# Performance work log

Measured on AMD Instinct MI355X. Metric: run time of the kernel, lower is better.

## Reference

```python
import jax, jax.numpy as jnp
import numpy as np

NEG_SLOPE = 0.2  # PyG GATConv default negative_slope
NUM_GRAPHS = 64
N, E, F_IN = 50000, 800000, 128


def _gat(x, src, dst, W, a_s, a_d, b, concat):
    # PyG GATConv: h = x W (per head); e_ij = leaky_relu(a_s.h_j + a_d.h_i);
    # softmax over incoming edges of each dst node; out_i = sum_j alpha_ij h_j
    n = x.shape[0]
    H, C = a_s.shape
    h = (x @ W).reshape(n, H, C)                     # [N,H,C]
    es = jnp.einsum('nhc,hc->nh', h, a_s)            # [N,H]
    ed = jnp.einsum('nhc,hc->nh', h, a_d)
    e = jax.nn.leaky_relu(es[src] + ed[dst], NEG_SLOPE)   # [E,H]
    m = jax.ops.segment_max(e, dst, num_segments=n)       # per-dst max (stable softmax)
    ex = jnp.exp(e - m[dst])
    den = jax.ops.segment_sum(ex, dst, num_segments=n)
    alpha = ex / den[dst]                                 # [E,H]
    out = jax.ops.segment_sum(h[src] * alpha[:, :, None], dst, num_segments=n)  # [N,H,C]
    if concat:
        return out.reshape(n, H * C) + b
    return out.mean(axis=1) + b


def setup_inputs() -> dict:
    key = jax.random.key(0)
    ks = jax.random.split(key, 10)
    x = jax.random.normal(ks[0], (N, F_IN), jnp.float32)
    edge_index = jax.random.randint(ks[1], (2, E), 0, N, dtype=jnp.int64)
    batch = jnp.sort(jax.random.randint(ks[2], (N,), 0, NUM_GRAPHS, dtype=jnp.int64))
    s1 = 1.0 / np.sqrt(F_IN)
    s2 = 1.0 / np.sqrt(256)
    return {
        'x': x,
        'edge_index': edge_index,
        'batch': batch,
        'W1': jax.random.normal(ks[3], (F_IN, 256), jnp.float32) * s1,
        'a_src1': jax.random.normal(ks[4], (4, 64), jnp.float32) * s2,
        'a_dst1': jax.random.normal(ks[5], (4, 64), jnp.float32) * s2,
        'b1': jnp.zeros((256,), jnp.float32),
        'W2': jax.random.normal(ks[6], (256, 128), jnp.float32) * s2,
        'a_src2': jax.random.normal(ks[7], (1, 128), jnp.float32) * (1.0 / np.sqrt(128)),
        'a_dst2': jax.random.normal(ks[8], (1, 128), jnp.float32) * (1.0 / np.sqrt(128)),
        'b2': jnp.zeros((128,), jnp.float32),
        'fc_w': jax.random.normal(ks[9], (128, 10), jnp.float32) * (1.0 / np.sqrt(128)),
        'fc_b': jnp.zeros((10,), jnp.float32),
    }


def reference(x, edge_index, batch, W1, a_src1, a_dst1, b1, W2, a_src2, a_dst2, b2, fc_w, fc_b):
    n = x.shape[0]
    loop = jnp.arange(n, dtype=edge_index.dtype)  # PyG add_self_loops=True
    src = jnp.concatenate([edge_index[0], loop])
    dst = jnp.concatenate([edge_index[1], loop])
    h = jax.nn.elu(_gat(x, src, dst, W1, a_src1, a_dst1, b1, True))   # dropout: eval mode -> identity
    h = jax.nn.elu(_gat(h, src, dst, W2, a_src2, a_dst2, b2, False))
    pooled = jax.ops.segment_sum(h, batch, num_segments=NUM_GRAPHS)
    cnt = jax.ops.segment_sum(jnp.ones((n,), h.dtype), batch, num_segments=NUM_GRAPHS)
    pooled = pooled / jnp.maximum(cnt, 1.0)[:, None]
    logits = pooled @ fc_w + fc_b
    return jax.nn.log_softmax(logits, axis=1)
```

## Files before the change

kernel.cpp:

```cpp
#include <hip/hip_runtime.h>
#include <math.h>

#define N_NODES 50000
#define N_PAD   50048
#define N_EDGES 800000
#define E_TOT   (N_EDGES + N_NODES)
#define NG 64
#define POOL_CHUNK 64
#define CAP 48
#define NBKT 512
#define BNODES 98
#define RCAP 24
#define FILL_CHUNK 2048
#define GEMM1_BLOCKS 3128
#define FILL_BLOCKS  391
#define PH1_DIAG (FILL_BLOCKS * 8)
#define PH1_TOTAL (GEMM1_BLOCKS + FILL_BLOCKS)

typedef short short8 __attribute__((ext_vector_type(8)));
typedef float floatx4 __attribute__((ext_vector_type(4)));
typedef float floatx2 __attribute__((ext_vector_type(2)));

__device__ inline short f2bf(float f) {
    union { float f; unsigned u; } v; v.f = f;
    unsigned r = v.u + 0x7fff + ((v.u >> 16) & 1);
    return (short)(r >> 16);
}
__device__ inline float bf2f(short s) {
    union { float f; unsigned u; } v;
    v.u = ((unsigned)(unsigned short)s) << 16;
    return v.f;
}

__device__ inline unsigned f2fp8(float f) {
    union { float f; unsigned u; } v; v.f = f;
    unsigned s = v.u & 0x80000000u;
    unsigned au = v.u & 0x7fffffffu;
    if (au > 0x43E00000u) au = 0x43E00000u;
    unsigned r = au + 0x7ffffu + ((au >> 20) & 1);
    int e8 = (int)(r >> 23) - 120;
    unsigned m3 = (r >> 20) & 7;
    unsigned code;
    if (e8 <= 0) code = 0;
    else if (e8 > 15) code = 0x7e;
    else code = ((unsigned)e8 << 3) | m3;
    return (s >> 24) | code;
}

__device__ inline float leaky_exp(float t) {
    t = t > 0.f ? t : 0.2f * t;
    return __expf(t);
}


__global__ __launch_bounds__(256) void phase1_kernel(const float* __restrict__ x,
                                                     const float* __restrict__ W1,
                                                     const float* __restrict__ a_s,
                                                     const float* __restrict__ a_d,
                                                     const int* __restrict__ ei,
                                                     unsigned short* __restrict__ gcnt,
                                                     unsigned* __restrict__ gb2,
                                                     unsigned char* __restrict__ C8,
                                                     float* __restrict__ es,
                                                     float* __restrict__ ed,
                                                     const float* __restrict__ W2,
                                                     const float* __restrict__ as2,
                                                     const float* __restrict__ ad2,
                                                     float* __restrict__ ws2,
                                                     float* __restrict__ wd2) {
    __shared__ short bs[64][136];
    __shared__ int hist[NBKT];
    int bid = blockIdx.x;
    int tid = threadIdx.x;

    if (bid == PH1_TOTAL) {
        int k = tid;
        float s = 0.f, d = 0.f;
        for (int c = 0; c < 128; c++) {
            float w = W2[k * 128 + c];
            s += w * as2[c];
            d += w * ad2[c];
        }
        ws2[k] = s;
        wd2[k] = d;
        return;
    }

    int gb = -1, fb = -1;
    if (bid < PH1_DIAG) {
        int g = bid >> 3, r = bid & 7;
        if (r == (g & 7)) fb = g;
        else gb = g * 7 + (r > (g & 7) ? r - 1 : r);
    } else {
        gb = (PH1_DIAG - FILL_BLOCKS) + (bid - PH1_DIAG);
    }

    if (fb >= 0) {
        hist[tid] = 0; hist[tid + 256] = 0;
        __syncthreads();
        unsigned meta[8], pay[8];
        int e0 = fb * FILL_CHUNK;
#pragma unroll
        for (int j = 0; j < 8; j++) {
            int t = e0 + j * 256 + tid;
            if (t < N_EDGES) {
                int s = ei[t];
                int d = ei[N_EDGES + t];
                unsigned bkt = (unsigned)d / 98u;
                int dlow = d - (int)bkt * 98;
                int pos = atomicAdd(&hist[bkt], 1);
                meta[j] = (bkt << 16) | (unsigned)pos;
                pay[j] = ((unsigned)s << 9) | (unsigned)dlow;
            } else {
                meta[j] = 0xffffffffu;
            }
        }
        __syncthreads();
        {
            int c0h = hist[tid];        if (c0h > RCAP) c0h = RCAP;
            int c1h = hist[tid + 256];  if (c1h > RCAP) c1h = RCAP;
            gcnt[fb * NBKT + tid] = (unsigned short)c0h;
            gcnt[fb * NBKT + tid + 256] = (unsigned short)c1h;
        }
#pragma unroll
        for (int j = 0; j < 8; j++) {
            if (meta[j] != 0xffffffffu) {
                unsigned bkt = meta[j] >> 16;
                unsigned pos = meta[j] & 0xffffu;
                if (pos < RCAP)
                    gb2[((size_t)bkt * FILL_BLOCKS + fb) * RCAP + pos] = pay[j];
            }
        }
        return;
    }

    const int K = 128, N = 256;
    int head = gb & 3;
    int bx = gb >> 2;
    int c0 = head * 64;

    int tc = tid & 63;
    int tk0 = (tid >> 6) * 32;
    for (int k = tk0; k < tk0 + 32; k++)
        bs[tc][k] = f2bf(W1[k * 256 + c0 + tc]);
    __syncthreads();

    int wid = tid >> 6;
    int lane = tid & 63;
    int m0 = bx * 64 + wid * 16;
    int mr = lane & 15;
    int quad = lane >> 4;
    int kq = quad << 3;
    int arow = m0 + mr; if (arow > N_NODES - 1) arow = N_NODES - 1;
    const float* aptr = x + (size_t)arow * K + kq;
    floatx4 acc[4] = {{0.f,0.f,0.f,0.f},{0.f,0.f,0.f,0.f},{0.f,0.f,0.f,0.f},{0.f,0.f,0.f,0.f}};
    for (int k0 = 0; k0 < K; k0 += 32) {
        float4 f0 = *(const float4*)(aptr + k0);
        float4 f1 = *(const float4*)(aptr + k0 + 4);
        short8 a;
        a[0] = f2bf(f0.x); a[1] = f2bf(f0.y); a[2] = f2bf(f0.z); a[3] = f2bf(f0.w);
        a[4] = f2bf(f1.x); a[5] = f2bf(f1.y); a[6] = f2bf(f1.z); a[7] = f2bf(f1.w);
#pragma unroll
        for (int t = 0; t < 4; t++) {
            short8 b = *(const short8*)&bs[t * 16 + mr][kq + k0];
            acc[t] = __builtin_amdgcn_mfma_f32_16x16x32_bf16(a, b, acc[t], 0, 0, 0);
        }
    }
    float asv[4], adv[4];
#pragma unroll
    for (int t = 0; t < 4; t++) {
        asv[t] = a_s[c0 + t * 16 + mr];
        adv[t] = a_d[c0 + t * 16 + mr];
    }
    int orow = m0 + (quad << 2);
#pragma unroll
    for (int r = 0; r < 4; r++) {
        float ps = acc[0][r] * asv[0] + acc[1][r] * asv[1] + acc[2][r] * asv[2] + acc[3][r] * asv[3];
        float pd = acc[0][r] * adv[0] + acc[1][r] * adv[1] + acc[2][r] * adv[2] + acc[3][r] * adv[3];
#pragma unroll
        for (int off = 8; off >= 1; off >>= 1) {
            ps += __shfl_xor(ps, off);
            pd += __shfl_xor(pd, off);
        }
        if (mr == 0) {
            es[(orow + r) * 4 + head] = ps;
            ed[(orow + r) * 4 + head] = pd;
        }
    }
#pragma unroll
    for (int t = 0; t < 4; t++) {
        int ocol = c0 + t * 16 + mr;
#pragma unroll
        for (int r = 0; r < 4; r++) {
            C8[(size_t)(orow + r) * N + ocol] = (unsigned char)f2fp8(acc[t][r]);
        }
    }
}


__global__ __launch_bounds__(512) void binfill_kernel(const unsigned* __restrict__ gb2,
                                                      const unsigned short* __restrict__ gcnt,
                                                      unsigned short* __restrict__ col,
                                                      int* __restrict__ degT) {
    __shared__ unsigned colL[BNODES * CAP / 2];
    __shared__ int cnt[BNODES];
    __shared__ unsigned short cl[FILL_BLOCKS + 1];
    int b = blockIdx.x, tid = threadIdx.x;
    int nbase = b * BNODES;

    for (int i = tid; i < BNODES * CAP / 8; i += 512) ((uint4*)colL)[i] = make_uint4(0, 0, 0, 0);
    if (tid < FILL_BLOCKS) cl[tid] = gcnt[tid * NBKT + b];
    if (tid < BNODES) cnt[tid] = (nbase + tid < N_NODES) ? 1 : 0;
    __syncthreads();

    if (tid < BNODES) {
        int nn = nbase + tid;
        if (nn < N_NODES) ((unsigned short*)colL)[tid * CAP] = (unsigned short)nn;
    }
    const uint4* src4 = (const uint4*)(gb2 + (size_t)b * FILL_BLOCKS * RCAP);
    for (int r = tid; r < FILL_BLOCKS * RCAP / 4; r += 512) {
        int blk = r / 6;
        int q = r - blk * 6;
        int c = cl[blk];
        if (q * 4 < c) {
            uint4 v = src4[r];
            unsigned vv[4] = {v.x, v.y, v.z, v.w};
#pragma unroll
            for (int j = 0; j < 4; j++) {
                if (q * 4 + j < c) {
                    unsigned p = vv[j];
                    int dlow = (int)(p & 511u);
                    int s = (int)(p >> 9);
                    int sp = atomicAdd(&cnt[dlow], 1);
                    if (sp < CAP) ((unsigned short*)colL)[dlow * CAP + sp] = (unsigned short)s;
                }
            }
        }
    }
    __syncthreads();

    uint4* cb = (uint4*)(col + (size_t)b * BNODES * CAP);
    for (int i = tid; i < BNODES * CAP / 8; i += 512) cb[i] = ((uint4*)colL)[i];
    if (tid < BNODES) {
        int nn = nbase + tid;
        if (nn < N_NODES) degT[nn] = cnt[tid];
    }
}


__global__ __launch_bounds__(256) void gather1_kernel(const unsigned char* __restrict__ h8,
                                                      const int* __restrict__ degT,
                                                      const unsigned short* __restrict__ col,
                                                      const float* __restrict__ es,
                                                      const float* __restrict__ ed,
                                                      const float* __restrict__ bias,
                                                      const float* __restrict__ ws2,
                                                      const float* __restrict__ wd2,
                                                      short* __restrict__ out,
                                                      float* __restrict__ es2,
                                                      float* __restrict__ ed2) {
    __shared__ float wlds[4][CAP * 4];
    __shared__ unsigned short ilds[4][CAP];
    int tid = threadIdx.x;
    int wid = tid >> 6;
    int n = __builtin_amdgcn_readfirstlane(blockIdx.x * 4 + wid);
    int l = tid & 63;
    int hh = l >> 4;
    int cnt = degT[n]; cnt = cnt < CAP ? cnt : CAP;
    int cnt8 = (cnt + 7) & ~7;

    if (l < cnt8) ilds[wid][l] = col[n * CAP + l];

    {
        int eA = l >> 2;
        int hA = l & 3;
        float edvA = ed[n * 4 + hA];
#pragma unroll
        for (int p = 0; p < 3; p++) {
            int e = p * 16 + eA;
            if (e < cnt8) {
                int s = ilds[wid][e];
                float w = (e < cnt) ? leaky_exp(es[s * 4 + hA] + edvA) : 0.f;
                wlds[wid][e * 4 + hA] = w;
            }
        }
    }

    float ax = 0.f, ay = 0.f, az = 0.f, aw = 0.f, den = 0.f;
    for (int eb = 0; eb < cnt8; eb += 8) {
        int idx[8];
#pragma unroll
        for (int j = 0; j < 8; j++) idx[j] = ilds[wid][eb + j];
        float wv[8];
#pragma unroll
        for (int j = 0; j < 8; j++) wv[j] = wlds[wid][(eb + j) * 4 + hh];
        unsigned hv[8];
#pragma unroll
        for (int j = 0; j < 8; j++)
            hv[j] = *(const unsigned*)&h8[(size_t)idx[j] * 256 + l * 4];
#pragma unroll
        for (int j = 0; j < 8; j++) {
            floatx2 lo = __builtin_amdgcn_cvt_pk_f32_fp8(hv[j], false);
            floatx2 hi = __builtin_amdgcn_cvt_pk_f32_fp8(hv[j], true);
            den += wv[j];
            ax += wv[j] * lo[0];
            ay += wv[j] * lo[1];
            az += wv[j] * hi[0];
            aw += wv[j] * hi[1];
        }
    }
    float inv = 1.0f / den;
    float4 bb = *(const float4*)&bias[l * 4];
    float o0 = ax * inv + bb.x;
    float o1 = ay * inv + bb.y;
    float o2 = az * inv + bb.z;
    float o3 = aw * inv + bb.w;
    o0 = o0 > 0.f ? o0 : __expf(o0) - 1.f;
    o1 = o1 > 0.f ? o1 : __expf(o1) - 1.f;
    o2 = o2 > 0.f ? o2 : __expf(o2) - 1.f;
    o3 = o3 > 0.f ? o3 : __expf(o3) - 1.f;
    short4 ob;
    ob.x = f2bf(o0); ob.y = f2bf(o1); ob.z = f2bf(o2); ob.w = f2bf(o3);
    *(short4*)&out[(size_t)n * 256 + l * 4] = ob;

    float4 s4 = *(const float4*)&ws2[l * 4];
    float4 d4 = *(const float4*)&wd2[l * 4];
    float ps = o0 * s4.x + o1 * s4.y + o2 * s4.z + o3 * s4.w;
    float pd = o0 * d4.x + o1 * d4.y + o2 * d4.z + o3 * d4.w;
#pragma unroll
    for (int off = 32; off >= 1; off >>= 1) {
        ps += __shfl_xor(ps, off);
        pd += __shfl_xor(pd, off);
    }
    if (l == 0) {
        es2[n] = ps;
        ed2[n] = pd;
    }
}


__global__ __launch_bounds__(256) void gemm2_kernel(const short* __restrict__ A,
                                                    const float* __restrict__ W2,
                                                    unsigned char* __restrict__ C8) {
    __shared__ short bs[64][264];
    const int K = 256, N = 128;
    int tid = threadIdx.x;
    int by = blockIdx.y;
    int c0 = by * 64;

    int tc = tid & 63;
    int tk0 = (tid >> 6) * 64;
    for (int k = tk0; k < tk0 + 64; k++)
        bs[tc][k] = f2bf(W2[k * 128 + c0 + tc]);
    __syncthreads();

    int wid = tid >> 6;
    int lane = tid & 63;
    int m0 = blockIdx.x * 64 + wid * 16;
    int mr = lane & 15;
    int quad = lane >> 4;
    int kq = quad << 3;
    const short* arow = A + (size_t)(m0 + mr) * K + kq;
    floatx4 acc[4] = {{0.f,0.f,0.f,0.f},{0.f,0.f,0.f,0.f},{0.f,0.f,0.f,0.f},{0.f,0.f,0.f,0.f}};
    for (int k0 = 0; k0 < K; k0 += 32) {
        short8 a = *(const short8*)(arow + k0);
#pragma unroll
        for (int t = 0; t < 4; t++) {
            short8 b = *(const short8*)&bs[t * 16 + mr][kq + k0];
            acc[t] = __builtin_amdgcn_mfma_f32_16x16x32_bf16(a, b, acc[t], 0, 0, 0);
        }
    }
    int orow = m0 + (quad << 2);
#pragma unroll
    for (int t = 0; t < 4; t++) {
        int ocol = c0 + t * 16 + mr;
#pragma unroll
        for (int r = 0; r < 4; r++) {
            C8[(size_t)(orow + r) * N + ocol] = (unsigned char)f2fp8(acc[t][r]);
        }
    }
}


__global__ __launch_bounds__(256) void gather2_kernel(const unsigned char* __restrict__ h8,
                                                      const int* __restrict__ deg,
                                                      const unsigned short* __restrict__ col,
                                                      const float* __restrict__ es2,
                                                      const float* __restrict__ ed2,
                                                      const float* __restrict__ bias,
                                                      short* __restrict__ out) {
    __shared__ float wlds[4][CAP];
    int tid = threadIdx.x;
    int wid = tid >> 6;
    int n = __builtin_amdgcn_readfirstlane(blockIdx.x * 4 + wid);
    int l = tid & 63;
    int cnt = deg[n]; cnt = cnt < CAP ? cnt : CAP;
    int cnt8 = (cnt + 7) & ~7;

    {
        float edv = ed2[n];
        if (l < cnt8) {
            int s = col[n * CAP + l];
            float w = (l < cnt) ? leaky_exp(es2[s] + edv) : 0.f;
            wlds[wid][l] = w;
        }
    }

    const unsigned int* cp = (const unsigned int*)(col + n * CAP);
    float ax = 0.f, ay = 0.f, den = 0.f;
    for (int eb = 0; eb < cnt8; eb += 8) {
        unsigned int cw0 = cp[(eb >> 1) + 0];
        unsigned int cw1 = cp[(eb >> 1) + 1];
        unsigned int cw2 = cp[(eb >> 1) + 2];
        unsigned int cw3 = cp[(eb >> 1) + 3];
        int idx[8];
        idx[0] = cw0 & 0xffff; idx[1] = cw0 >> 16;
        idx[2] = cw1 & 0xffff; idx[3] = cw1 >> 16;
        idx[4] = cw2 & 0xffff; idx[5] = cw2 >> 16;
        idx[6] = cw3 & 0xffff; idx[7] = cw3 >> 16;
        float wv[8];
#pragma unroll
        for (int j = 0; j < 8; j++) wv[j] = wlds[wid][eb + j];
        unsigned hv[8];
#pragma unroll
        for (int j = 0; j < 8; j++)
            hv[j] = *(const unsigned short*)&h8[(size_t)idx[j] * 128 + l * 2];
#pragma unroll
        for (int j = 0; j < 8; j++) {
            floatx2 lo = __builtin_amdgcn_cvt_pk_f32_fp8(hv[j], false);
            den += wv[j];
            ax += wv[j] * lo[0];
            ay += wv[j] * lo[1];
        }
    }
    float inv = 1.0f / den;
    float2 bb = *(const float2*)&bias[l * 2];
    float o0 = ax * inv + bb.x;
    float o1 = ay * inv + bb.y;
    o0 = o0 > 0.f ? o0 : __expf(o0) - 1.f;
    o1 = o1 > 0.f ? o1 : __expf(o1) - 1.f;
    short2 ob;
    ob.x = f2bf(o0); ob.y = f2bf(o1);
    *(short2*)&out[(size_t)n * 128 + l * 2] = ob;
}


__global__ __launch_bounds__(128) void pool1_kernel(const short* __restrict__ h,
                                                    const int* __restrict__ batch,
                                                    float* __restrict__ pooled) {
    int c = threadIdx.x;
    int n0 = blockIdx.x * POOL_CHUNK;
    int n1 = n0 + POOL_CHUNK;
    if (n1 > N_NODES) n1 = N_NODES;
    if (n0 >= n1) return;
    float acc = 0.f;
    int g = batch[n0];
    for (int n = n0; n < n1; n++) {
        int bg = batch[n];
        if (bg != g) {
            atomicAdd(&pooled[g * 128 + c], acc);
            acc = 0.f;
            g = bg;
        }
        acc += bf2f(h[n * 128 + c]);
    }
    atomicAdd(&pooled[g * 128 + c], acc);
}


__global__ void fc_kernel(const float* __restrict__ pooled, const int* __restrict__ batch,
                          const float* __restrict__ fcw, const float* __restrict__ fcb,
                          float* __restrict__ out) {
    int g = threadIdx.x;
    if (g >= NG) return;
    int lo = 0, hi = N_NODES;
    while (lo < hi) {
        int mid = (lo + hi) >> 1;
        if (batch[mid] < g) lo = mid + 1; else hi = mid;
    }
    int start = lo;
    lo = start; hi = N_NODES;
    while (lo < hi) {
        int mid = (lo + hi) >> 1;
        if (batch[mid] <= g) lo = mid + 1; else hi = mid;
    }
    int cnt = lo - start;
    float inv = 1.0f / (float)(cnt > 0 ? cnt : 1);

    float lg[10];
#pragma unroll
    for (int j = 0; j < 10; j++) lg[j] = fcb[j];
    for (int k = 0; k < 128; k++) {
        float p = pooled[g * 128 + k] * inv;
#pragma unroll
        for (int j = 0; j < 10; j++) lg[j] += p * fcw[k * 10 + j];
    }
    float m = lg[0];
#pragma unroll
    for (int j = 1; j < 10; j++) m = fmaxf(m, lg[j]);
    float se = 0.f;
#pragma unroll
    for (int j = 0; j < 10; j++) se += __expf(lg[j] - m);
    float lse = m + __logf(se);
#pragma unroll
    for (int j = 0; j < 10; j++) out[g * 10 + j] = lg[j] - lse;
}


extern "C" void kernel_launch(void* const* d_in, const int* in_sizes, int n_in,
                              void* d_out, int out_size, void* d_ws, size_t ws_size,
                              hipStream_t stream) {
    const float* x     = (const float*)d_in[0];
    const int*   ei    = (const int*)d_in[1];
    const int*   batch = (const int*)d_in[2];
    const float* W1    = (const float*)d_in[3];
    const float* as1   = (const float*)d_in[4];
    const float* ad1   = (const float*)d_in[5];
    const float* b1    = (const float*)d_in[6];
    const float* W2    = (const float*)d_in[7];
    const float* as2   = (const float*)d_in[8];
    const float* ad2   = (const float*)d_in[9];
    const float* b2    = (const float*)d_in[10];
    const float* fcw   = (const float*)d_in[11];
    const float* fcb   = (const float*)d_in[12];
    float* out = (float*)d_out;

    char* ws = (char*)d_ws;
    size_t off = 0;
    auto alloc = [&](size_t bytes) -> void* {
        void* p = ws + off;
        off = (off + bytes + 255) & ~(size_t)255;
        return p;
    };
    float* pooled        = (float*)alloc(NG * 128 * 4);
    int* degT            = (int*)alloc((size_t)N_PAD * 4);
    unsigned short* col  = (unsigned short*)alloc((size_t)NBKT * BNODES * CAP * 2);
    unsigned* gb2        = (unsigned*)alloc((size_t)NBKT * FILL_BLOCKS * RCAP * 4);
    unsigned short* gcnt = (unsigned short*)alloc((size_t)FILL_BLOCKS * NBKT * 2);
    float* es1           = (float*)alloc((size_t)N_PAD * 4 * 4);
    float* ed1           = (float*)alloc((size_t)N_PAD * 4 * 4);
    float* es2           = (float*)alloc((size_t)N_PAD * 4);
    float* ed2           = (float*)alloc((size_t)N_PAD * 4);
    float* ws2           = (float*)alloc(256 * 4);
    float* wd2           = (float*)alloc(256 * 4);
    unsigned char* h1    = (unsigned char*)alloc((size_t)N_PAD * 256);
    short* h1p           = (short*)alloc((size_t)N_PAD * 256 * 2);
    unsigned char* h2    = (unsigned char*)alloc((size_t)N_PAD * 128);
    short* h2p           = (short*)alloc((size_t)N_PAD * 128 * 2);

    hipMemsetAsync(pooled, 0, (size_t)NG * 128 * 4, stream);

    int ngrid = N_NODES / 4;

    phase1_kernel<<<PH1_TOTAL + 1, 256, 0, stream>>>(x, W1, as1, ad1, ei, gcnt, gb2, h1, es1, ed1,
                                                     W2, as2, ad2, ws2, wd2);
    binfill_kernel<<<NBKT, 512, 0, stream>>>(gb2, gcnt, col, degT);
    gather1_kernel<<<ngrid, 256, 0, stream>>>(h1, degT, col, es1, ed1, b1, ws2, wd2,
                                              h1p, es2, ed2);
    gemm2_kernel<<<dim3(N_PAD / 64, 2), 256, 0, stream>>>(h1p, W2, h2);
    gather2_kernel<<<ngrid, 256, 0, stream>>>(h2, degT, col, es2, ed2, b2, h2p);

    pool1_kernel<<<(N_NODES + POOL_CHUNK - 1) / POOL_CHUNK, 128, 0, stream>>>(h2p, batch, pooled);
    fc_kernel<<<1, 64, 0, stream>>>(pooled, batch, fcw, fcb, out);
}
```

Measured before the change: 237.9 us.

## Fuse mean-pool into gather2 and loop heads inside GEMM blocks

Layer-2 aggregation now accumulates per-graph sums directly, with a small LDS reduction and atomics into the pooled buffer. This removes the bf16 h2p intermediate, the separate pool kernel and the memset, whose zeroing moves into phase1's spare block. GEMM1 and GEMM2 blocks now load their A tile once and loop over heads or column halves, so the activations are read once instead of four or two times. The cost is fewer GEMM blocks, repeated W staging with extra barriers, and a gather2 where each wave handles eight nodes in sequence.

```diff
diff --git a/kernel.cpp b/kernel.cpp
--- a/kernel.cpp
+++ b/kernel.cpp
@@ -6,16 +6,15 @@
 #define N_EDGES 800000
 #define E_TOT   (N_EDGES + N_NODES)
 #define NG 64
-#define POOL_CHUNK 64
 #define CAP 48
 #define NBKT 512
 #define BNODES 98
 #define RCAP 24
 #define FILL_CHUNK 2048
-#define GEMM1_BLOCKS 3128
+#define GEMM1_BLOCKS 782
 #define FILL_BLOCKS  391
-#define PH1_DIAG (FILL_BLOCKS * 8)
 #define PH1_TOTAL (GEMM1_BLOCKS + FILL_BLOCKS)
+#define G2_NB 32
 
 typedef short short8 __attribute__((ext_vector_type(8)));
 typedef float floatx4 __attribute__((ext_vector_type(4)));
@@ -25,11 +24,6 @@
     union { float f; unsigned u; } v; v.f = f;
     unsigned r = v.u + 0x7fff + ((v.u >> 16) & 1);
     return (short)(r >> 16);
-}
-__device__ inline float bf2f(short s) {
-    union { float f; unsigned u; } v;
-    v.u = ((unsigned)(unsigned short)s) << 16;
-    return v.f;
 }
 
 __device__ inline unsigned f2fp8(float f) {
@@ -67,7 +61,8 @@
                                                      const float* __restrict__ as2,
                                                      const float* __restrict__ ad2,
                                                      float* __restrict__ ws2,
-                                                     float* __restrict__ wd2) {
+                                                     float* __restrict__ wd2,
+                                                     float* __restrict__ pooled) {
     __shared__ short bs[64][136];
     __shared__ int hist[NBKT];
     int bid = blockIdx.x;
@@ -83,16 +78,15 @@
         }
         ws2[k] = s;
         wd2[k] = d;
+        for (int i = tid; i < NG * 128; i += 256) pooled[i] = 0.f;
         return;
     }
 
     int gb = -1, fb = -1;
-    if (bid < PH1_DIAG) {
-        int g = bid >> 3, r = bid & 7;
-        if (r == (g & 7)) fb = g;
-        else gb = g * 7 + (r > (g & 7) ? r - 1 : r);
-    } else {
-        gb = (PH1_DIAG - FILL_BLOCKS) + (bid - PH1_DIAG);
+    {
+        int g3 = bid / 3, r3 = bid - g3 * 3;
+        if (r3 == 2) fb = g3;
+        else         gb = g3 * 2 + r3;
     }
 
     if (fb >= 0) {
@@ -135,64 +129,67 @@
     }
 
     const int K = 128, N = 256;
-    int head = gb & 3;
-    int bx = gb >> 2;
-    int c0 = head * 64;
-
     int tc = tid & 63;
-    int tk0 = (tid >> 6) * 32;
-    for (int k = tk0; k < tk0 + 32; k++)
-        bs[tc][k] = f2bf(W1[k * 256 + c0 + tc]);
-    __syncthreads();
-
+    int tk0s = (tid >> 6) * 32;
     int wid = tid >> 6;
     int lane = tid & 63;
-    int m0 = bx * 64 + wid * 16;
+    int m0 = gb * 64 + wid * 16;
     int mr = lane & 15;
     int quad = lane >> 4;
     int kq = quad << 3;
     int arow = m0 + mr; if (arow > N_NODES - 1) arow = N_NODES - 1;
     const float* aptr = x + (size_t)arow * K + kq;
-    floatx4 acc[4] = {{0.f,0.f,0.f,0.f},{0.f,0.f,0.f,0.f},{0.f,0.f,0.f,0.f},{0.f,0.f,0.f,0.f}};
-    for (int k0 = 0; k0 < K; k0 += 32) {
-        float4 f0 = *(const float4*)(aptr + k0);
-        float4 f1 = *(const float4*)(aptr + k0 + 4);
-        short8 a;
-        a[0] = f2bf(f0.x); a[1] = f2bf(f0.y); a[2] = f2bf(f0.z); a[3] = f2bf(f0.w);
-        a[4] = f2bf(f1.x); a[5] = f2bf(f1.y); a[6] = f2bf(f1.z); a[7] = f2bf(f1.w);
+    short8 a[4];
+#pragma unroll
+    for (int kk = 0; kk < 4; kk++) {
+        float4 f0 = *(const float4*)(aptr + kk * 32);
+        float4 f1 = *(const float4*)(aptr + kk * 32 + 4);
+        a[kk][0] = f2bf(f0.x); a[kk][1] = f2bf(f0.y); a[kk][2] = f2bf(f0.z); a[kk][3] = f2bf(f0.w);
+        a[kk][4] = f2bf(f1.x); a[kk][5] = f2bf(f1.y); a[kk][6] = f2bf(f1.z); a[kk][7] = f2bf(f1.w);
+    }
+    int orow = m0 + (quad << 2);
+    for (int head = 0; head < 4; head++) {
+        int c0 = head * 64;
+        if (head) __syncthreads();
+        for (int k = tk0s; k < tk0s + 32; k++)
+            bs[tc][k] = f2bf(W1[k * 256 + c0 + tc]);
+        __syncthreads();
+        floatx4 acc[4] = {{0.f,0.f,0.f,0.f},{0.f,0.f,0.f,0.f},{0.f,0.f,0.f,0.f},{0.f,0.f,0.f,0.f}};
+#pragma unroll
+        for (int kk = 0; kk < 4; kk++) {
+#pragma unroll
+            for (int t = 0; t < 4; t++) {
+                short8 b = *(const short8*)&bs[t * 16 + mr][kq + kk * 32];
+                acc[t] = __builtin_amdgcn_mfma_f32_16x16x32_bf16(a[kk], b, acc[t], 0, 0, 0);
+            }
+        }
+        float asv[4], adv[4];
 #pragma unroll
         for (int t = 0; t < 4; t++) {
-            short8 b = *(const short8*)&bs[t * 16 + mr][kq + k0];
-            acc[t] = __builtin_amdgcn_mfma_f32_16x16x32_bf16(a, b, acc[t], 0, 0, 0);
-        }
-    }
-    float asv[4], adv[4];
-#pragma unroll
-    for (int t = 0; t < 4; t++) {
-        asv[t] = a_s[c0 + t * 16 + mr];
-        adv[t] = a_d[c0 + t * 16 + mr];
-    }
-    int orow = m0 + (quad << 2);
-#pragma unroll
-    for (int r = 0; r < 4; r++) {
-        float ps = acc[0][r] * asv[0] + acc[1][r] * asv[1] + acc[2][r] * asv[2] + acc[3][r] * asv[3];
-        float pd = acc[0][r] * adv[0] + acc[1][r] * adv[1] + acc[2][r] * adv[2] + acc[3][r] * adv[3];
-#pragma unroll
-        for (int off = 8; off >= 1; off >>= 1) {
-            ps += __shfl_xor(ps, off);
-            pd += __shfl_xor(pd, off);
-        }
-        if (mr == 0) {
-            es[(orow + r) * 4 + head] = ps;
-            ed[(orow + r) * 4 + head] = pd;
-        }
-    }
-#pragma unroll
-    for (int t = 0; t < 4; t++) {
-        int ocol = c0 + t * 16 + mr;
+            asv[t] = a_s[c0 + t * 16 + mr];
+            adv[t] = a_d[c0 + t * 16 + mr];
+        }
 #pragma unroll
         for (int r = 0; r < 4; r++) {
-            C8[(size_t)(orow + r) * N + ocol] = (unsigned char)f2fp8(acc[t][r]);
+            float ps = acc[0][r] * asv[0] + acc[1][r] * asv[1] + acc[2][r] * asv[2] + acc[3][r] * asv[3];
+            float pd = acc[0][r] * adv[0] + acc[1][r] * adv[1] + acc[2][r] * adv[2] + acc[3][r] * adv[3];
+#pragma unroll
+            for (int off = 8; off >= 1; off >>= 1) {
+                ps += __shfl_xor(ps, off);
+                pd += __shfl_xor(pd, off);
+            }
+            if (mr == 0) {
+                es[(orow + r) * 4 + head] = ps;
+                ed[(orow + r) * 4 + head] = pd;
+            }
+        }
+#pragma unroll
+        for (int t = 0; t < 4; t++) {
+            int ocol = c0 + t * 16 + mr;
+#pragma unroll
+            for (int r = 0; r < 4; r++) {
+                C8[(size_t)(orow + r) * N + ocol] = (unsigned char)f2fp8(acc[t][r]);
+            }
         }
     }
 }
@@ -345,15 +342,8 @@
     __shared__ short bs[64][264];
     const int K = 256, N = 128;
     int tid = threadIdx.x;
-    int by = blockIdx.y;
-    int c0 = by * 64;
-
     int tc = tid & 63;
-    int tk0 = (tid >> 6) * 64;
-    for (int k = tk0; k < tk0 + 64; k++)
-        bs[tc][k] = f2bf(W2[k * 128 + c0 + tc]);
-    __syncthreads();
-
+    int tk0s = (tid >> 6) * 64;
     int wid = tid >> 6;
     int lane = tid & 63;
     int m0 = blockIdx.x * 64 + wid * 16;
@@ -361,22 +351,32 @@
     int quad = lane >> 4;
     int kq = quad << 3;
     const short* arow = A + (size_t)(m0 + mr) * K + kq;
-    floatx4 acc[4] = {{0.f,0.f,0.f,0.f},{0.f,0.f,0.f,0.f},{0.f,0.f,0.f,0.f},{0.f,0.f,0.f,0.f}};
-    for (int k0 = 0; k0 < K; k0 += 32) {
-        short8 a = *(const short8*)(arow + k0);
+    short8 a[8];
+#pragma unroll
+    for (int kk = 0; kk < 8; kk++) a[kk] = *(const short8*)(arow + kk * 32);
+    int orow = m0 + (quad << 2);
+    for (int by = 0; by < 2; by++) {
+        int c0 = by * 64;
+        if (by) __syncthreads();
+        for (int k = tk0s; k < tk0s + 64; k++)
+            bs[tc][k] = f2bf(W2[k * 128 + c0 + tc]);
+        __syncthreads();
+        floatx4 acc[4] = {{0.f,0.f,0.f,0.f},{0.f,0.f,0.f,0.f},{0.f,0.f,0.f,0.f},{0.f,0.f,0.f,0.f}};
+#pragma unroll
+        for (int kk = 0; kk < 8; kk++) {
+#pragma unroll
+            for (int t = 0; t < 4; t++) {
+                short8 b = *(const short8*)&bs[t * 16 + mr][kq + kk * 32];
+                acc[t] = __builtin_amdgcn_mfma_f32_16x16x32_bf16(a[kk], b, acc[t], 0, 0, 0);
+            }
+        }
 #pragma unroll
         for (int t = 0; t < 4; t++) {
-            short8 b = *(const short8*)&bs[t * 16 + mr][kq + k0];
-            acc[t] = __builtin_amdgcn_mfma_f32_16x16x32_bf16(a, b, acc[t], 0, 0, 0);
-        }
-    }
-    int orow = m0 + (quad << 2);
-#pragma unroll
-    for (int t = 0; t < 4; t++) {
-        int ocol = c0 + t * 16 + mr;
-#pragma unroll
-        for (int r = 0; r < 4; r++) {
-            C8[(size_t)(orow + r) * N + ocol] = (unsigned char)f2fp8(acc[t][r]);
+            int ocol = c0 + t * 16 + mr;
+#pragma unroll
+            for (int r = 0; r < 4; r++) {
+                C8[(size_t)(orow + r) * N + ocol] = (unsigned char)f2fp8(acc[t][r]);
+            }
         }
     }
 }
@@ -388,83 +388,107 @@
                                                       const float* __restrict__ es2,
                                                       const float* __restrict__ ed2,
                                                       const float* __restrict__ bias,
-                                                      short* __restrict__ out) {
+                                                      const int* __restrict__ batch,
+                                                      float* __restrict__ pooled) {
     __shared__ float wlds[4][CAP];
+    __shared__ float plds[8][128];
+    __shared__ int pg[8];
+    __shared__ int pcnt;
     int tid = threadIdx.x;
     int wid = tid >> 6;
-    int n = __builtin_amdgcn_readfirstlane(blockIdx.x * 4 + wid);
     int l = tid & 63;
-    int cnt = deg[n]; cnt = cnt < CAP ? cnt : CAP;
-    int cnt8 = (cnt + 7) & ~7;
-
-    {
-        float edv = ed2[n];
-        if (l < cnt8) {
-            int s = col[n * CAP + l];
-            float w = (l < cnt) ? leaky_exp(es2[s] + edv) : 0.f;
-            wlds[wid][l] = w;
-        }
-    }
-
-    const unsigned int* cp = (const unsigned int*)(col + n * CAP);
-    float ax = 0.f, ay = 0.f, den = 0.f;
-    for (int eb = 0; eb < cnt8; eb += 8) {
-        unsigned int cw0 = cp[(eb >> 1) + 0];
-        unsigned int cw1 = cp[(eb >> 1) + 1];
-        unsigned int cw2 = cp[(eb >> 1) + 2];
-        unsigned int cw3 = cp[(eb >> 1) + 3];
-        int idx[8];
-        idx[0] = cw0 & 0xffff; idx[1] = cw0 >> 16;
-        idx[2] = cw1 & 0xffff; idx[3] = cw1 >> 16;
-        idx[4] = cw2 & 0xffff; idx[5] = cw2 >> 16;
-        idx[6] = cw3 & 0xffff; idx[7] = cw3 >> 16;
-        float wv[8];
-#pragma unroll
-        for (int j = 0; j < 8; j++) wv[j] = wlds[wid][eb + j];
-        unsigned hv[8];
-#pragma unroll
-        for (int j = 0; j < 8; j++)
-            hv[j] = *(const unsigned short*)&h8[(size_t)idx[j] * 128 + l * 2];
-#pragma unroll
-        for (int j = 0; j < 8; j++) {
-            floatx2 lo = __builtin_amdgcn_cvt_pk_f32_fp8(hv[j], false);
-            den += wv[j];
-            ax += wv[j] * lo[0];
-            ay += wv[j] * lo[1];
-        }
-    }
-    float inv = 1.0f / den;
-    float2 bb = *(const float2*)&bias[l * 2];
-    float o0 = ax * inv + bb.x;
-    float o1 = ay * inv + bb.y;
-    o0 = o0 > 0.f ? o0 : __expf(o0) - 1.f;
-    o1 = o1 > 0.f ? o1 : __expf(o1) - 1.f;
-    short2 ob;
-    ob.x = f2bf(o0); ob.y = f2bf(o1);
-    *(short2*)&out[(size_t)n * 128 + l * 2] = ob;
-}
-
-
-__global__ __launch_bounds__(128) void pool1_kernel(const short* __restrict__ h,
-                                                    const int* __restrict__ batch,
-                                                    float* __restrict__ pooled) {
-    int c = threadIdx.x;
-    int n0 = blockIdx.x * POOL_CHUNK;
-    int n1 = n0 + POOL_CHUNK;
-    if (n1 > N_NODES) n1 = N_NODES;
-    if (n0 >= n1) return;
-    float acc = 0.f;
-    int g = batch[n0];
-    for (int n = n0; n < n1; n++) {
-        int bg = batch[n];
-        if (bg != g) {
-            atomicAdd(&pooled[g * 128 + c], acc);
-            acc = 0.f;
-            g = bg;
-        }
-        acc += bf2f(h[n * 128 + c]);
-    }
-    atomicAdd(&pooled[g * 128 + c], acc);
+    if (tid == 0) pcnt = 0;
+    __syncthreads();
+
+    int c0 = l * 2;
+    float2 bb = *(const float2*)&bias[c0];
+    int nbase = blockIdx.x * G2_NB + wid * (G2_NB / 4);
+    int curg = -1;
+    float a0 = 0.f, a1 = 0.f;
+
+    auto flush = [&]() {
+        if (curg >= 0) {
+            int idx = 0;
+            if (l == 0) idx = atomicAdd(&pcnt, 1);
+            idx = __shfl(idx, 0);
+            if (idx < 8) {
+                if (l == 0) pg[idx] = curg;
+                plds[idx][c0] = a0;
+                plds[idx][c0 + 1] = a1;
+            } else {
+                atomicAdd(&pooled[curg * 128 + c0], a0);
+                atomicAdd(&pooled[curg * 128 + c0 + 1], a1);
+            }
+        }
+    };
+
+    for (int i = 0; i < G2_NB / 4; i++) {
+        int n = nbase + i;
+        if (n < N_NODES) {
+            int bg = batch[n];
+            if (bg != curg) {
+                flush();
+                curg = bg; a0 = 0.f; a1 = 0.f;
+            }
+            int cnt = deg[n]; cnt = cnt < CAP ? cnt : CAP;
+            int cnt8 = (cnt + 7) & ~7;
+            float edv = ed2[n];
+            if (l < cnt8) {
+                int s = col[n * CAP + l];
+                float w = (l < cnt) ? leaky_exp(es2[s] + edv) : 0.f;
+                wlds[wid][l] = w;
+            }
+            const unsigned int* cp = (const unsigned int*)(col + n * CAP);
+            float ax = 0.f, ay = 0.f, den = 0.f;
+            for (int eb = 0; eb < cnt8; eb += 8) {
+                unsigned int cw0 = cp[(eb >> 1) + 0];
+                unsigned int cw1 = cp[(eb >> 1) + 1];
+                unsigned int cw2 = cp[(eb >> 1) + 2];
+                unsigned int cw3 = cp[(eb >> 1) + 3];
+                int idx[8];
+                idx[0] = cw0 & 0xffff; idx[1] = cw0 >> 16;
+                idx[2] = cw1 & 0xffff; idx[3] = cw1 >> 16;
+                idx[4] = cw2 & 0xffff; idx[5] = cw2 >> 16;
+                idx[6] = cw3 & 0xffff; idx[7] = cw3 >> 16;
+                float wv[8];
+#pragma unroll
+                for (int j = 0; j < 8; j++) wv[j] = wlds[wid][eb + j];
+                unsigned hv[8];
+#pragma unroll
+                for (int j = 0; j < 8; j++)
+                    hv[j] = *(const unsigned short*)&h8[(size_t)idx[j] * 128 + l * 2];
+#pragma unroll
+                for (int j = 0; j < 8; j++) {
+                    floatx2 lo = __builtin_amdgcn_cvt_pk_f32_fp8(hv[j], false);
+                    den += wv[j];
+                    ax += wv[j] * lo[0];
+                    ay += wv[j] * lo[1];
+                }
+            }
+            float inv = 1.0f / den;
+            float o0 = ax * inv + bb.x;
+            float o1 = ay * inv + bb.y;
+            o0 = o0 > 0.f ? o0 : __expf(o0) - 1.f;
+            o1 = o1 > 0.f ? o1 : __expf(o1) - 1.f;
+            a0 += o0; a1 += o1;
+        }
+    }
+    flush();
+    __syncthreads();
+
+    int m = pcnt; if (m > 8) m = 8;
+    if (tid < 128) {
+        for (int e = 0; e < m; e++) {
+            int ge = pg[e];
+            bool first = true;
+            for (int e2 = 0; e2 < e; e2++) if (pg[e2] == ge) first = false;
+            if (first) {
+                float s = plds[e][tid];
+                for (int e3 = e + 1; e3 < m; e3++) if (pg[e3] == ge) s += plds[e3][tid];
+                atomicAdd(&pooled[ge * 128 + tid], s);
+            }
+        }
+    }
 }
 
 
@@ -546,20 +570,14 @@
     unsigned char* h1    = (unsigned char*)alloc((size_t)N_PAD * 256);
     short* h1p           = (short*)alloc((size_t)N_PAD * 256 * 2);
     unsigned char* h2    = (unsigned char*)alloc((size_t)N_PAD * 128);
-    short* h2p           = (short*)alloc((size_t)N_PAD * 128 * 2);
-
-    hipMemsetAsync(pooled, 0, (size_t)NG * 128 * 4, stream);
-
-    int ngrid = N_NODES / 4;
 
     phase1_kernel<<<PH1_TOTAL + 1, 256, 0, stream>>>(x, W1, as1, ad1, ei, gcnt, gb2, h1, es1, ed1,
-                                                     W2, as2, ad2, ws2, wd2);
+                                                     W2, as2, ad2, ws2, wd2, pooled);
     binfill_kernel<<<NBKT, 512, 0, stream>>>(gb2, gcnt, col, degT);
-    gather1_kernel<<<ngrid, 256, 0, stream>>>(h1, degT, col, es1, ed1, b1, ws2, wd2,
-                                              h1p, es2, ed2);
-    gemm2_kernel<<<dim3(N_PAD / 64, 2), 256, 0, stream>>>(h1p, W2, h2);
-    gather2_kernel<<<ngrid, 256, 0, stream>>>(h2, degT, col, es2, ed2, b2, h2p);
-
-    pool1_kernel<<<(N_NODES + POOL_CHUNK - 1) / POOL_CHUNK, 128, 0, stream>>>(h2p, batch, pooled);
+    gather1_kernel<<<N_NODES / 4, 256, 0, stream>>>(h1, degT, col, es1, ed1, b1, ws2, wd2,
+                                                    h1p, es2, ed2);
+    gemm2_kernel<<<N_PAD / 64, 256, 0, stream>>>(h1p, W2, h2);
+    gather2_kernel<<<(N_NODES + G2_NB - 1) / G2_NB, 256, 0, stream>>>(h2, degT, col, es2, ed2, b2,
+                                                                      batch, pooled);
     fc_kernel<<<1, 64, 0, stream>>>(pooled, batch, fcw, fcb, out);
 }
```

Result: faster. 231.8 us (-2.6%).
